# Kernel optimization log

Hardware: AMD Instinct MI355X
Metric: run time of the kernel (lower is better)

Reference implementation:

```python
import jax, jax.numpy as jnp
import numpy as np

N_NODES = 100000
N_EDGES = 3200000
D_FEAT = 512
HIDDEN = 16
N_CLASSES = 7


def setup_inputs() -> dict:
    key = jax.random.key(0)
    k1, k2, k3, k4 = jax.random.split(key, 4)
    x = jax.random.normal(k1, (N_NODES, D_FEAT), dtype=jnp.float32)
    edge_index = jax.random.randint(k2, (2, N_EDGES), 0, N_NODES, dtype=jnp.int64)
    # Glorot-ish scaled weights
    W1 = jax.random.normal(k3, (D_FEAT, HIDDEN), dtype=jnp.float32) * (1.0 / np.sqrt(D_FEAT))
    b1 = jnp.zeros((HIDDEN,), dtype=jnp.float32)
    W2 = jax.random.normal(k4, (HIDDEN, N_CLASSES), dtype=jnp.float32) * (1.0 / np.sqrt(HIDDEN))
    b2 = jnp.zeros((N_CLASSES,), dtype=jnp.float32)
    return {"x": x, "edge_index": edge_index, "W1": W1, "b1": b1, "W2": W2, "b2": b2}


def _gcn_norm(edge_index, num_nodes):
    # Add self-loops, then symmetric normalization: D^-1/2 A D^-1/2
    loop = jnp.arange(num_nodes, dtype=edge_index.dtype)
    src = jnp.concatenate([edge_index[0], loop])
    dst = jnp.concatenate([edge_index[1], loop])
    deg = jax.ops.segment_sum(jnp.ones_like(dst, dtype=jnp.float32), dst,
                              num_segments=num_nodes)
    dinv = jnp.where(deg > 0, jax.lax.rsqrt(deg), 0.0)
    w = dinv[src] * dinv[dst]  # [E+N]
    return src, dst, w


def _gcn_conv(x, W, b, src, dst, w, num_nodes):
    h = x @ W                               # transform first (small out dim)
    m = jax.ops.segment_sum(h[src] * w[:, None], dst, num_segments=num_nodes)
    return m + b


def reference(x, edge_index, W1, b1, W2, b2):
    n = x.shape[0]
    src, dst, w = _gcn_norm(edge_index, n)
    h = jax.nn.relu(_gcn_conv(x, W1, b1, src, dst, w, n))
    # dropout is identity at inference
    logits = _gcn_conv(h, W2, b2, src, dst, w, n)
    return jax.nn.log_softmax(logits, axis=1)
```

## Files before the change

kernel.cpp:

```cpp
#include <hip/hip_runtime.h>
#include <cmath>

#define N_NODES   100000
#define N_EDGES   3200000
#define D_FEAT    512
#define HIDDEN    16
#define N_CLASSES 7

#define NCHUNK 250
#define CHUNK  12800
#define NBKT   1563
#define BCAP   2560

typedef __attribute__((ext_vector_type(4))) float  f32x4;
typedef __attribute__((ext_vector_type(8))) short  bf16x8;

__device__ __forceinline__ short f2bf(float f) {
    union { float f; unsigned u; } v; v.f = f;
    unsigned r = v.u + 0x7fffu + ((v.u >> 16) & 1u);
    return (short)(r >> 16);
}
__device__ __forceinline__ float bf2f(unsigned short s) {
    union { unsigned u; float f; } v; v.u = ((unsigned)s) << 16;
    return v.f;
}

__global__ __launch_bounds__(1024) void k_scatterD(const int* __restrict__ src,
                                                   const int* __restrict__ dst,
                                                   unsigned* __restrict__ cnt,
                                                   unsigned* __restrict__ packed) {
    __shared__ unsigned h[NBKT];
    int t = threadIdx.x, b = blockIdx.x;
    for (int i = t; i < NBKT; i += 1024) h[i] = 0u;
    __syncthreads();
    int base = b * CHUNK;
    #pragma unroll 2
    for (int k = 0; k < 13; ++k) {
        int idx = k * 1024 + t;
        if (idx < CHUNK) atomicAdd(&h[((unsigned)dst[base + idx]) >> 6], 1u);
    }
    __syncthreads();
    for (int i = t; i < NBKT; i += 1024) {
        unsigned c = h[i];
        h[i] = c ? ((unsigned)i * BCAP + atomicAdd(&cnt[i], c)) : 0u;
    }
    __syncthreads();
    #pragma unroll 2
    for (int k = 0; k < 13; ++k) {
        int idx = k * 1024 + t;
        if (idx < CHUNK) {
            int e = base + idx;
            unsigned d = (unsigned)dst[e];
            unsigned pos = atomicAdd(&h[d >> 6], 1u);
            packed[pos] = ((d & 63u) << 24) | (unsigned)src[e];
        }
    }
}

__global__ __launch_bounds__(256) void k_bucket(const unsigned* __restrict__ packed,
                                                const unsigned* __restrict__ cnt,
                                                unsigned* __restrict__ deg,
                                                unsigned* __restrict__ row_start,
                                                float* __restrict__ dinv,
                                                int* __restrict__ csr_src) {
    __shared__ unsigned hh[4][64], sc[64], cur[64];
    int t = threadIdx.x, b = blockIdx.x;
    int w = t >> 6, l = t & 63;
    unsigned rs = (unsigned)b * BCAP;
    unsigned re = rs + cnt[b];
    hh[w][l] = 0u;
    __syncthreads();
    for (unsigned i = rs + t; i < re; i += 256)
        atomicAdd(&hh[w][packed[i] >> 24], 1u);
    __syncthreads();
    unsigned total = 0u;
    if (t < 64) {
        total = hh[0][t] + hh[1][t] + hh[2][t] + hh[3][t];
        sc[t] = total;
    }
    __syncthreads();
    #pragma unroll
    for (int off = 1; off < 64; off <<= 1) {
        unsigned add = (t >= off && t < 64) ? sc[t - off] : 0u;
        __syncthreads();
        if (t < 64) sc[t] += add;
        __syncthreads();
    }
    if (t < 64) {
        unsigned excl = sc[t] - total;
        int node = b * 64 + t;
        if (node < N_NODES) {
            deg[node]       = total;
            row_start[node] = rs + excl;
            dinv[node]      = rsqrtf((float)(total + 1u));
        }
        cur[t] = rs + excl;
    }
    __syncthreads();
    for (unsigned i = rs + t; i < re; i += 256) {
        unsigned p = packed[i];
        unsigned pos = atomicAdd(&cur[p >> 24], 1u);
        csr_src[pos] = (int)(p & 0xFFFFFFu);
    }
}

__global__ __launch_bounds__(256) void k_gemm1(const float* __restrict__ x,
                                               const float* __restrict__ w1,
                                               const float* __restrict__ dinv,
                                               unsigned short* __restrict__ h1p) {
    __shared__ __align__(16) short w1t[16][520];
    int tid = threadIdx.x;
    for (int idx = tid; idx < D_FEAT * HIDDEN; idx += 256) {
        int k = idx >> 4, n = idx & 15;
        w1t[n][k] = f2bf(w1[idx]);
    }
    __syncthreads();

    int lane = tid & 63, wid = tid >> 6;
    int m  = lane & 15;
    int kg = lane >> 4;

    bf16x8 bfrag[16];
    #pragma unroll
    for (int ks = 0; ks < 16; ++ks)
        bfrag[ks] = *(const bf16x8*)&w1t[m][ks * 32 + kg * 8];

    int tile = blockIdx.x * 4 + wid;
    if (tile >= (N_NODES / 16)) return;

    const f32x4* xr = (const f32x4*)(x + (size_t)(tile * 16 + m) * D_FEAT);
    f32x4 acc = {0.f, 0.f, 0.f, 0.f};
    #pragma unroll
    for (int ks = 0; ks < 16; ++ks) {
        f32x4 x0 = xr[ks * 8 + kg * 2];
        f32x4 x1 = xr[ks * 8 + kg * 2 + 1];
        bf16x8 a;
        a[0] = f2bf(x0[0]); a[1] = f2bf(x0[1]); a[2] = f2bf(x0[2]); a[3] = f2bf(x0[3]);
        a[4] = f2bf(x1[0]); a[5] = f2bf(x1[1]); a[6] = f2bf(x1[2]); a[7] = f2bf(x1[3]);
        acc = __builtin_amdgcn_mfma_f32_16x16x32_bf16(a, bfrag[ks], acc, 0, 0, 0);
    }
    size_t base = (size_t)tile * 256;
    #pragma unroll
    for (int r = 0; r < 4; ++r) {
        int rr = kg * 4 + r;
        h1p[base + rr * 16 + m] = (unsigned short)f2bf(dinv[tile * 16 + rr] * acc[r]);
    }
}

__global__ __launch_bounds__(256) void k_gather1(const int* __restrict__ csr_src,
                                                 const unsigned* __restrict__ row_start,
                                                 const unsigned* __restrict__ deg,
                                                 const unsigned short* __restrict__ h1p,
                                                 const float* __restrict__ dinv,
                                                 const float* __restrict__ w2,
                                                 const float* __restrict__ b1,
                                                 float* __restrict__ h2p) {
    __shared__ float w2s[16][8];
    __shared__ float b1s[16];
    int tid  = threadIdx.x;
    if (tid < 128) {
        int jj = tid >> 3, c = tid & 7;
        w2s[jj][c] = (c < N_CLASSES) ? w2[jj * N_CLASSES + c] : 0.f;
    }
    if (tid < 16) b1s[tid] = b1[tid];
    __syncthreads();

    int lane = tid & 63;
    int node = blockIdx.x * 4 + (tid >> 6);
    int j  = lane & 15;
    int sl = lane >> 4;

    unsigned start = row_start[node];
    unsigned end   = start + deg[node];

    float acc = (sl == 0) ? bf2f(h1p[(size_t)node * 16 + j]) : 0.f;
    unsigned e = start;
    for (; e + 16 <= end; e += 16) {
        int s0 = csr_src[e      + sl];
        int s1 = csr_src[e + 4  + sl];
        int s2 = csr_src[e + 8  + sl];
        int s3 = csr_src[e + 12 + sl];
        float v0 = bf2f(h1p[(size_t)s0 * 16 + j]);
        float v1 = bf2f(h1p[(size_t)s1 * 16 + j]);
        float v2 = bf2f(h1p[(size_t)s2 * 16 + j]);
        float v3 = bf2f(h1p[(size_t)s3 * 16 + j]);
        acc += v0; acc += v1; acc += v2; acc += v3;
    }
    for (; e < end; e += 4) {
        unsigned idx = e + (unsigned)sl;
        float v = 0.f;
        if (idx < end) v = bf2f(h1p[(size_t)csr_src[idx] * 16 + j]);
        acc += v;
    }
    acc += __shfl_down(acc, 32);
    acc += __shfl_down(acc, 16);

    float di = dinv[node];
    float hv = fmaxf(fmaf(di, acc, b1s[j]), 0.f);
    float o = 0.f;
    int c = lane & 7;
    #pragma unroll
    for (int jj = 0; jj < 16; ++jj)
        o = fmaf(__shfl(hv, jj), w2s[jj][c], o);
    if (lane < 8)
        h2p[(size_t)node * 8 + c] = (c < N_CLASSES) ? di * o : 0.f;
}

__global__ __launch_bounds__(256) void k_gather2(const int* __restrict__ csr_src,
                                                 const unsigned* __restrict__ row_start,
                                                 const unsigned* __restrict__ deg,
                                                 const float* __restrict__ dinv,
                                                 const float* __restrict__ h2p,
                                                 const float* __restrict__ b2,
                                                 float* __restrict__ out) {
    int tid  = threadIdx.x;
    int lane = tid & 63;
    int node = blockIdx.x * 4 + (tid >> 6);
    int j  = lane & 7;
    int sl = lane >> 3;

    unsigned start = row_start[node];
    unsigned end   = start + deg[node];

    float acc = (sl == 0) ? h2p[(size_t)node * 8 + j] : 0.f;
    unsigned e = start;
    for (; e + 32 <= end; e += 32) {
        int s0 = csr_src[e      + sl];
        int s1 = csr_src[e + 8  + sl];
        int s2 = csr_src[e + 16 + sl];
        int s3 = csr_src[e + 24 + sl];
        float v0 = h2p[(size_t)s0 * 8 + j];
        float v1 = h2p[(size_t)s1 * 8 + j];
        float v2 = h2p[(size_t)s2 * 8 + j];
        float v3 = h2p[(size_t)s3 * 8 + j];
        acc += v0; acc += v1; acc += v2; acc += v3;
    }
    for (; e < end; e += 8) {
        unsigned idx = e + (unsigned)sl;
        float v = 0.f;
        if (idx < end) v = h2p[(size_t)csr_src[idx] * 8 + j];
        acc += v;
    }
    acc += __shfl_down(acc, 32);
    acc += __shfl_down(acc, 16);
    acc += __shfl_down(acc, 8);
    float di = dinv[node];
    float logit = (j < N_CLASSES) ? di * acc + b2[j] : -1e30f;
    float mx = logit;
    #pragma unroll
    for (int mk = 1; mk < 8; mk <<= 1) mx = fmaxf(mx, __shfl_xor(mx, mk, 8));
    float ex = (j < N_CLASSES) ? __expf(logit - mx) : 0.f;
    float sum = ex;
    #pragma unroll
    for (int mk = 1; mk < 8; mk <<= 1) sum += __shfl_xor(sum, mk, 8);
    if (sl == 0 && j < N_CLASSES)
        out[(size_t)node * N_CLASSES + j] = logit - mx - __logf(sum);
}

extern "C" void kernel_launch(void* const* d_in, const int* in_sizes, int n_in,
                              void* d_out, int out_size, void* d_ws, size_t ws_size,
                              hipStream_t stream) {
    const float* x  = (const float*)d_in[0];
    const int*   ei = (const int*)d_in[1];
    const float* w1 = (const float*)d_in[2];
    const float* b1 = (const float*)d_in[3];
    const float* w2 = (const float*)d_in[4];
    const float* b2 = (const float*)d_in[5];
    float* out = (float*)d_out;

    const int* src = ei;
    const int* dst = ei + N_EDGES;

    unsigned* w32            = (unsigned*)d_ws;
    float*    dinv           = (float*)(w32 + 0);
    unsigned short* h1p      = (unsigned short*)(w32 + 102400);
    float*    h2p            = (float*)(w32 + 902400);
    unsigned* deg            = w32 + 1702400;
    unsigned* row_start      = w32 + 1804800;
    unsigned* cnt            = w32 + 1907200;
    unsigned* packed         = w32 + 1909248;
    int*      csr_src        = (int*)(w32 + 5910528);

    const int GB = (N_NODES / 16 + 3) / 4;

    hipMemsetAsync(cnt, 0, NBKT * sizeof(unsigned), stream);
    k_scatterD<<<NCHUNK, 1024, 0, stream>>>(src, dst, cnt, packed);
    k_bucket  <<<NBKT,   256,  0, stream>>>(packed, cnt, deg, row_start, dinv, csr_src);
    k_gemm1   <<<GB,     256,  0, stream>>>(x, w1, dinv, h1p);
    k_gather1 <<<25000,  256,  0, stream>>>(csr_src, row_start, deg, h1p, dinv, w2, b1, h2p);
    k_gather2 <<<25000,  256,  0, stream>>>(csr_src, row_start, deg, dinv, h2p, b2, out);
}
```

Baseline: 487.4 us.

## Vectorize gathers with 16-byte row loads and shrink scatter chunk size

The two neighbor-gather kernels are restructured so that each pair of lanes loads a whole feature row with 16-byte vector loads, one edge per lane pair, 32 edges per iteration. Previously each lane loaded a single scalar element. Per-feature partial sums are reduced with xor shuffles and the halves are exchanged. The final linear layer and the log-softmax are then computed redundantly in each lane. Separately, the scatter kernel uses smaller chunks (625 blocks of 5120 edges) with fully unrolled, bounds-free loops. This raises parallelism at the cost of more global counter atomics.

```diff
diff --git a/kernel.cpp b/kernel.cpp
--- a/kernel.cpp
+++ b/kernel.cpp
@@ -7,8 +7,8 @@
 #define HIDDEN    16
 #define N_CLASSES 7
 
-#define NCHUNK 250
-#define CHUNK  12800
+#define NCHUNK 625
+#define CHUNK  5120
 #define NBKT   1563
 #define BCAP   2560
 
@@ -23,6 +23,12 @@
 __device__ __forceinline__ float bf2f(unsigned short s) {
     union { unsigned u; float f; } v; v.u = ((unsigned)s) << 16;
     return v.f;
+}
+__device__ __forceinline__ float bflo(unsigned u) {
+    union { unsigned u; float f; } v; v.u = u << 16; return v.f;
+}
+__device__ __forceinline__ float bfhi(unsigned u) {
+    union { unsigned u; float f; } v; v.u = u & 0xFFFF0000u; return v.f;
 }
 
 __global__ __launch_bounds__(1024) void k_scatterD(const int* __restrict__ src,
@@ -34,26 +40,21 @@
     for (int i = t; i < NBKT; i += 1024) h[i] = 0u;
     __syncthreads();
     int base = b * CHUNK;
-    #pragma unroll 2
-    for (int k = 0; k < 13; ++k) {
-        int idx = k * 1024 + t;
-        if (idx < CHUNK) atomicAdd(&h[((unsigned)dst[base + idx]) >> 6], 1u);
-    }
+    #pragma unroll
+    for (int k = 0; k < 5; ++k)
+        atomicAdd(&h[((unsigned)dst[base + k * 1024 + t]) >> 6], 1u);
     __syncthreads();
     for (int i = t; i < NBKT; i += 1024) {
         unsigned c = h[i];
         h[i] = c ? ((unsigned)i * BCAP + atomicAdd(&cnt[i], c)) : 0u;
     }
     __syncthreads();
-    #pragma unroll 2
-    for (int k = 0; k < 13; ++k) {
-        int idx = k * 1024 + t;
-        if (idx < CHUNK) {
-            int e = base + idx;
-            unsigned d = (unsigned)dst[e];
-            unsigned pos = atomicAdd(&h[d >> 6], 1u);
-            packed[pos] = ((d & 63u) << 24) | (unsigned)src[e];
-        }
+    #pragma unroll
+    for (int k = 0; k < 5; ++k) {
+        int e = base + k * 1024 + t;
+        unsigned d = (unsigned)dst[e];
+        unsigned pos = atomicAdd(&h[d >> 6], 1u);
+        packed[pos] = ((d & 63u) << 24) | (unsigned)src[e];
     }
 }
 
@@ -167,41 +168,53 @@
 
     int lane = tid & 63;
     int node = blockIdx.x * 4 + (tid >> 6);
-    int j  = lane & 15;
-    int sl = lane >> 4;
+    int half = lane & 1;
+    int slot = lane >> 1;
 
     unsigned start = row_start[node];
     unsigned end   = start + deg[node];
 
-    float acc = (sl == 0) ? bf2f(h1p[(size_t)node * 16 + j]) : 0.f;
-    unsigned e = start;
-    for (; e + 16 <= end; e += 16) {
-        int s0 = csr_src[e      + sl];
-        int s1 = csr_src[e + 4  + sl];
-        int s2 = csr_src[e + 8  + sl];
-        int s3 = csr_src[e + 12 + sl];
-        float v0 = bf2f(h1p[(size_t)s0 * 16 + j]);
-        float v1 = bf2f(h1p[(size_t)s1 * 16 + j]);
-        float v2 = bf2f(h1p[(size_t)s2 * 16 + j]);
-        float v3 = bf2f(h1p[(size_t)s3 * 16 + j]);
-        acc += v0; acc += v1; acc += v2; acc += v3;
-    }
-    for (; e < end; e += 4) {
-        unsigned idx = e + (unsigned)sl;
-        float v = 0.f;
-        if (idx < end) v = bf2f(h1p[(size_t)csr_src[idx] * 16 + j]);
-        acc += v;
-    }
-    acc += __shfl_down(acc, 32);
-    acc += __shfl_down(acc, 16);
+    float acc[8] = {0,0,0,0,0,0,0,0};
+    uint4 sv = *(const uint4*)(h1p + (size_t)node * 16 + half * 8);
+    if (lane < 2) {
+        acc[0] += bflo(sv.x); acc[1] += bfhi(sv.x);
+        acc[2] += bflo(sv.y); acc[3] += bfhi(sv.y);
+        acc[4] += bflo(sv.z); acc[5] += bfhi(sv.z);
+        acc[6] += bflo(sv.w); acc[7] += bfhi(sv.w);
+    }
+    for (unsigned e0 = start; e0 < end; e0 += 32) {
+        unsigned idx = e0 + (unsigned)slot;
+        if (idx < end) {
+            int s = csr_src[idx];
+            uint4 rv = *(const uint4*)(h1p + (size_t)s * 16 + half * 8);
+            acc[0] += bflo(rv.x); acc[1] += bfhi(rv.x);
+            acc[2] += bflo(rv.y); acc[3] += bfhi(rv.y);
+            acc[4] += bflo(rv.z); acc[5] += bfhi(rv.z);
+            acc[6] += bflo(rv.w); acc[7] += bfhi(rv.w);
+        }
+    }
+    #pragma unroll
+    for (int mk = 2; mk <= 32; mk <<= 1) {
+        #pragma unroll
+        for (int k = 0; k < 8; ++k) acc[k] += __shfl_xor(acc[k], mk);
+    }
+    float oth[8];
+    #pragma unroll
+    for (int k = 0; k < 8; ++k) oth[k] = __shfl_xor(acc[k], 1);
 
     float di = dinv[node];
-    float hv = fmaxf(fmaf(di, acc, b1s[j]), 0.f);
+    float h[16];
+    #pragma unroll
+    for (int k = 0; k < 8; ++k) {
+        float glo = half ? oth[k] : acc[k];
+        float ghi = half ? acc[k] : oth[k];
+        h[k]     = fmaxf(fmaf(di, glo, b1s[k]),     0.f);
+        h[k + 8] = fmaxf(fmaf(di, ghi, b1s[k + 8]), 0.f);
+    }
+    int c = lane & 7;
     float o = 0.f;
-    int c = lane & 7;
-    #pragma unroll
-    for (int jj = 0; jj < 16; ++jj)
-        o = fmaf(__shfl(hv, jj), w2s[jj][c], o);
+    #pragma unroll
+    for (int j = 0; j < 16; ++j) o = fmaf(h[j], w2s[j][c], o);
     if (lane < 8)
         h2p[(size_t)node * 8 + c] = (c < N_CLASSES) ? di * o : 0.f;
 }
@@ -216,45 +229,56 @@
     int tid  = threadIdx.x;
     int lane = tid & 63;
     int node = blockIdx.x * 4 + (tid >> 6);
-    int j  = lane & 7;
-    int sl = lane >> 3;
+    int half = lane & 1;
+    int slot = lane >> 1;
 
     unsigned start = row_start[node];
     unsigned end   = start + deg[node];
 
-    float acc = (sl == 0) ? h2p[(size_t)node * 8 + j] : 0.f;
-    unsigned e = start;
-    for (; e + 32 <= end; e += 32) {
-        int s0 = csr_src[e      + sl];
-        int s1 = csr_src[e + 8  + sl];
-        int s2 = csr_src[e + 16 + sl];
-        int s3 = csr_src[e + 24 + sl];
-        float v0 = h2p[(size_t)s0 * 8 + j];
-        float v1 = h2p[(size_t)s1 * 8 + j];
-        float v2 = h2p[(size_t)s2 * 8 + j];
-        float v3 = h2p[(size_t)s3 * 8 + j];
-        acc += v0; acc += v1; acc += v2; acc += v3;
-    }
-    for (; e < end; e += 8) {
-        unsigned idx = e + (unsigned)sl;
-        float v = 0.f;
-        if (idx < end) v = h2p[(size_t)csr_src[idx] * 8 + j];
-        acc += v;
-    }
-    acc += __shfl_down(acc, 32);
-    acc += __shfl_down(acc, 16);
-    acc += __shfl_down(acc, 8);
+    float acc[4] = {0, 0, 0, 0};
+    f32x4 sv = *(const f32x4*)(h2p + (size_t)node * 8 + half * 4);
+    if (lane < 2) { acc[0] += sv[0]; acc[1] += sv[1]; acc[2] += sv[2]; acc[3] += sv[3]; }
+    for (unsigned e0 = start; e0 < end; e0 += 32) {
+        unsigned idx = e0 + (unsigned)slot;
+        if (idx < end) {
+            int s = csr_src[idx];
+            f32x4 rv = *(const f32x4*)(h2p + (size_t)s * 8 + half * 4);
+            acc[0] += rv[0]; acc[1] += rv[1]; acc[2] += rv[2]; acc[3] += rv[3];
+        }
+    }
+    #pragma unroll
+    for (int mk = 2; mk <= 32; mk <<= 1) {
+        #pragma unroll
+        for (int k = 0; k < 4; ++k) acc[k] += __shfl_xor(acc[k], mk);
+    }
+    float oth[4];
+    #pragma unroll
+    for (int k = 0; k < 4; ++k) oth[k] = __shfl_xor(acc[k], 1);
+
+    float l[8];
+    #pragma unroll
+    for (int k = 0; k < 4; ++k) {
+        l[k]     = half ? oth[k] : acc[k];
+        l[k + 4] = half ? acc[k] : oth[k];
+    }
     float di = dinv[node];
-    float logit = (j < N_CLASSES) ? di * acc + b2[j] : -1e30f;
-    float mx = logit;
-    #pragma unroll
-    for (int mk = 1; mk < 8; mk <<= 1) mx = fmaxf(mx, __shfl_xor(mx, mk, 8));
-    float ex = (j < N_CLASSES) ? __expf(logit - mx) : 0.f;
-    float sum = ex;
-    #pragma unroll
-    for (int mk = 1; mk < 8; mk <<= 1) sum += __shfl_xor(sum, mk, 8);
-    if (sl == 0 && j < N_CLASSES)
-        out[(size_t)node * N_CLASSES + j] = logit - mx - __logf(sum);
+    float lg[N_CLASSES];
+    float mx = -1e30f;
+    #pragma unroll
+    for (int cc = 0; cc < N_CLASSES; ++cc) {
+        lg[cc] = fmaf(di, l[cc], b2[cc]);
+        mx = fmaxf(mx, lg[cc]);
+    }
+    float sum = 0.f;
+    #pragma unroll
+    for (int cc = 0; cc < N_CLASSES; ++cc) sum += __expf(lg[cc] - mx);
+    float lse = mx + __logf(sum);
+    if (lane < N_CLASSES) {
+        float v = lg[0];
+        #pragma unroll
+        for (int cc = 1; cc < N_CLASSES; ++cc) if (lane == cc) v = lg[cc];
+        out[(size_t)node * N_CLASSES + lane] = v - lse;
+    }
 }
 
 extern "C" void kernel_launch(void* const* d_in, const int* in_sizes, int n_in,
```

Measured after the change: 496.5 us. Within noise of the previous version (+1.9%).
